# Kernel tuning notes

Hardware: AMD Instinct MI355X
Metric: run time of the kernel (lower is better)

## Reference

```python
import jax, jax.numpy as jnp
import numpy as np

B, N, D = 4, 1024, 1024
H = 16
RS, RC = 32, 32
MLP = int(D * 4.0)
EPS = 1e-6


def _ln(x):
    # LayerNorm with no scale/bias (flax defaults: eps=1e-6)
    m = jnp.mean(x, axis=-1, keepdims=True)
    v = jnp.mean(jnp.square(x - m), axis=-1, keepdims=True)
    return (x - m) * jax.lax.rsqrt(v + EPS)


def _rms(x, scale):
    rms = jnp.sqrt(jnp.mean(jnp.square(x), axis=-1, keepdims=True) + EPS)
    return scale * x / rms


def _modulate(x, shift, scale):
    return x * (1 + scale[:, None]) + shift[:, None]


def setup_inputs() -> dict:
    key = jax.random.key(0)
    ks = jax.random.split(key, 20)
    s = 0.02
    return {
        'x': jax.random.normal(ks[0], (B, N, D), jnp.float32),
        'c': jax.random.normal(ks[1], (B, D), jnp.float32),
        'cls_token': jax.random.normal(ks[2], (B, D), jnp.float32),
        'Wc': jax.random.normal(ks[3], (D, 6 * D), jnp.float32) * s,
        'bc': jax.random.normal(ks[4], (6 * D,), jnp.float32) * s,
        'Wqkv': jax.random.normal(ks[5], (D, 3 * D), jnp.float32) * s,
        'bqkv': jnp.zeros((3 * D,), jnp.float32),
        'Wo': jax.random.normal(ks[6], (D, D), jnp.float32) * s,
        'bo': jnp.zeros((D,), jnp.float32),
        'A_s': jax.random.normal(ks[7], (D, RS), jnp.float32) * s,
        'B_s': jax.random.normal(ks[8], (RS, D), jnp.float32) * s,
        'rms_s_scale': jnp.ones((D,), jnp.float32),
        'C_r': jax.random.normal(ks[9], (D, RC), jnp.float32) * s,
        'D_r': jax.random.normal(ks[10], (RC, D), jnp.float32) * s,
        'rms_c_scale': jnp.ones((D,), jnp.float32),
        'W1': jax.random.normal(ks[11], (D, MLP), jnp.float32) * s,
        'b1': jnp.zeros((MLP,), jnp.float32),
        'W2': jax.random.normal(ks[12], (MLP, D), jnp.float32) * s,
        'b2': jnp.zeros((D,), jnp.float32),
    }


def reference(x, c, cls_token, Wc, bc, Wqkv, bqkv, Wo, bo, A_s, B_s,
              rms_s_scale, C_r, D_r, rms_c_scale, W1, b1, W2, b2):
    hd = D // H
    # AdaLN conditioning
    c_proj = jax.nn.silu(c) @ Wc + bc                    # (B, 6D)
    shift_a, scale_a, gate_a, shift_m, scale_m, gate_m = jnp.split(c_proj, 6, axis=-1)

    # Self-attention branch
    x_norm = _modulate(_ln(x), shift_a, scale_a)         # (B, N, D)
    qkv = x_norm @ Wqkv + bqkv                           # (B, N, 3D)
    q, k, v = jnp.split(qkv, 3, axis=-1)
    q = q.reshape(B, N, H, hd).transpose(0, 2, 1, 3)     # (B, H, N, hd)
    k = k.reshape(B, N, H, hd).transpose(0, 2, 1, 3)
    v = v.reshape(B, N, H, hd).transpose(0, 2, 1, 3)
    attn_w = jax.nn.softmax(jnp.einsum('bhqd,bhkd->bhqk', q, k) * hd ** (-0.5), axis=-1)
    attn_out = jnp.einsum('bhqk,bhkd->bhqd', attn_w, v)
    attn_out = attn_out.transpose(0, 2, 1, 3).reshape(B, N, D)
    attn_out = attn_out @ Wo + bo
    Y = x + gate_a[:, None] * attn_out

    # Self-gram low-rank branch (residual)
    gram_s = (x @ A_s) @ B_s                             # (B, N, D)
    X_prime = _rms(gram_s, rms_s_scale) + Y

    # Cross-gram branch via CLS token (no residual)
    u_c = cls_token[:, :, None] * C_r[None]              # (B, D, RC)
    v_c = jnp.einsum('bnd,bdr->bnr', X_prime, u_c)       # (B, N, RC)
    gram_c = v_c @ D_r                                   # (B, N, D)
    Z = _rms(gram_c, rms_c_scale)

    # MLP branch
    z_norm = _modulate(_ln(Z), shift_m, scale_m)
    h = jax.nn.gelu(z_norm @ W1 + b1) @ W2 + b2
    return Z + gate_m[:, None] * h
```

## Files before the change

kernel.cpp:

```cpp
#include <hip/hip_runtime.h>
#include <stdint.h>

typedef float  f32x4  __attribute__((ext_vector_type(4)));
typedef int    i32x4  __attribute__((ext_vector_type(4)));
typedef __bf16 bf16x4 __attribute__((ext_vector_type(4)));

#define D_    1024
#define SIXD  6144
#define QSCALE 0.18033688011112042f

#define BAR() asm volatile("s_barrier" ::: "memory")

__device__ __forceinline__ void mfma16(const i32x4 &a, const i32x4 &b, f32x4 &c) {
  asm("v_mfma_f32_16x16x32_bf16 %0, %1, %2, %0" : "+v"(c) : "v"(a), "v"(b));
}
__device__ __forceinline__ void mfma16a(const i32x4 &a, const i32x4 &b, f32x4 &c) {
  asm("v_mfma_f32_16x16x32_bf16 %0, %1, %2, %0" : "+a"(c) : "v"(a), "v"(b));
}

__device__ __forceinline__ void gload_lds16(const void* g, void* l) {
  __builtin_amdgcn_global_load_lds(
      (const __attribute__((address_space(1))) uint32_t*)g,
      (__attribute__((address_space(3))) uint32_t*)l, 16, 0, 0);
}

__global__ __launch_bounds__(256)
void cond_gemm(const float* __restrict__ c, const float* __restrict__ Wc,
               const float* __restrict__ bc, float* __restrict__ cproj)
{
  __shared__ float sc[4096];
  __shared__ float tp[8][4][32];
  int tid = threadIdx.x;
  for (int i = tid; i < 4096; i += 256) {
    float v = c[i];
    sc[i] = v / (1.f + __expf(-v));
  }
  __syncthreads();
  int colo = tid & 31, kseg = tid >> 5;
  int col = blockIdx.x * 32 + colo;
  float a0 = 0.f, a1 = 0.f, a2 = 0.f, a3 = 0.f;
  for (int k = kseg * 128; k < kseg * 128 + 128; k++) {
    float w = Wc[(size_t)k * SIXD + col];
    a0 += sc[k] * w; a1 += sc[1024 + k] * w;
    a2 += sc[2048 + k] * w; a3 += sc[3072 + k] * w;
  }
  tp[kseg][0][colo] = a0; tp[kseg][1][colo] = a1;
  tp[kseg][2][colo] = a2; tp[kseg][3][colo] = a3;
  __syncthreads();
  if (kseg == 0) {
#pragma unroll
    for (int b = 0; b < 4; b++) {
      float s = bc[col];
#pragma unroll
      for (int g = 0; g < 8; g++) s += tp[g][b][colo];
      cproj[b * SIXD + col] = s;
    }
  }
}

__global__ __launch_bounds__(256)
void transpose_all(const float* __restrict__ Wqkv, const float* __restrict__ Wo,
                   const float* __restrict__ W1, const float* __restrict__ W2,
                   __bf16* __restrict__ Wqkvt, __bf16* __restrict__ Wot,
                   __bf16* __restrict__ W1t, __bf16* __restrict__ W2t)
{
  __shared__ __bf16 t[64][65];
  int bid = blockIdx.x;
  const float* W; __bf16* Wt; int Kdim, Ndim, lb;
  if (bid < 768)       { W = Wqkv; Wt = Wqkvt; Kdim = 1024; Ndim = 3072; lb = bid; }
  else if (bid < 1024) { W = Wo;   Wt = Wot;   Kdim = 1024; Ndim = 1024; lb = bid - 768; }
  else if (bid < 2048) { W = W1;   Wt = W1t;   Kdim = 1024; Ndim = 4096; lb = bid - 1024; }
  else                 { W = W2;   Wt = W2t;   Kdim = 4096; Ndim = 1024; lb = bid - 2048; }
  int ntn = Ndim >> 6;
  int kt = lb / ntn, nt = lb % ntn;
  int tid = threadIdx.x;
  const float* src = W + (size_t)(kt * 64) * Ndim + nt * 64;
#pragma unroll
  for (int i = 0; i < 4; i++) {
    int k = i * 16 + (tid >> 4);
    int c4 = tid & 15;
    float4 v = ((const float4*)(src + (size_t)k * Ndim))[c4];
    t[k][c4 * 4 + 0] = (__bf16)v.x; t[k][c4 * 4 + 1] = (__bf16)v.y;
    t[k][c4 * 4 + 2] = (__bf16)v.z; t[k][c4 * 4 + 3] = (__bf16)v.w;
  }
  __syncthreads();
  __bf16* dst = Wt + (size_t)(nt * 64) * Kdim + kt * 64;
  int n = tid >> 2, ks = (tid & 3) * 16;
  bf16x4 o0, o1, o2, o3;
#pragma unroll
  for (int j = 0; j < 4; j++) {
    o0[j] = t[ks + j][n];      o1[j] = t[ks + 4 + j][n];
    o2[j] = t[ks + 8 + j][n];  o3[j] = t[ks + 12 + j][n];
  }
  __bf16* dp = dst + (size_t)n * Kdim + ks;
  *(bf16x4*)(dp) = o0; *(bf16x4*)(dp + 4) = o1;
  *(bf16x4*)(dp + 8) = o2; *(bf16x4*)(dp + 12) = o3;
}

__global__ __launch_bounds__(256)
void transpose_v(const __bf16* __restrict__ qkv, __bf16* __restrict__ Vt)
{
  __shared__ __bf16 t[32][33];
  int bid = blockIdx.x;
  int dt = bid & 1, nt = (bid >> 1) & 31, bh = bid >> 6;
  int b = bh >> 4, h = bh & 15;
  int x = threadIdx.x & 31, yq = threadIdx.x >> 5;
  const __bf16* src = qkv + ((size_t)(b * 1024 + nt * 32)) * 3072 + 2048 + h * 64 + dt * 32;
#pragma unroll
  for (int i = 0; i < 4; i++) {
    int row = yq * 4 + i;
    t[row][x] = src[(size_t)row * 3072 + x];
  }
  __syncthreads();
  __bf16* dst = Vt + ((size_t)(bh * 64 + dt * 32)) * 1024 + nt * 32;
#pragma unroll
  for (int i = 0; i < 4; i++) {
    int drow = yq * 4 + i;
    dst[(size_t)drow * 1024 + x] = t[x][drow];
  }
}

__global__ __launch_bounds__(256)
void ln_mod(const float* __restrict__ X, const float* __restrict__ cproj,
            int shift_off, int scale_off, __bf16* __restrict__ Out)
{
  int row = blockIdx.x;
  int b = row >> 10;
  int tid = threadIdx.x;
  const float4* xr = (const float4*)(X + (size_t)row * D_);
  float4 v = xr[tid];
  float s  = v.x + v.y + v.z + v.w;
  float s2 = v.x * v.x + v.y * v.y + v.z * v.z + v.w * v.w;
#pragma unroll
  for (int off = 1; off < 64; off <<= 1) {
    s  += __shfl_xor(s,  off, 64);
    s2 += __shfl_xor(s2, off, 64);
  }
  __shared__ float red[8];
  int wave = tid >> 6, lane = tid & 63;
  if (lane == 0) { red[wave] = s; red[4 + wave] = s2; }
  __syncthreads();
  s  = red[0] + red[1] + red[2] + red[3];
  s2 = red[4] + red[5] + red[6] + red[7];
  float mean = s * (1.f / D_);
  float var  = s2 * (1.f / D_) - mean * mean;
  float rstd = rsqrtf(var + 1e-6f);
  const float4* sh = (const float4*)(cproj + b * SIXD + shift_off);
  const float4* sc = (const float4*)(cproj + b * SIXD + scale_off);
  float4 shv = sh[tid], scv = sc[tid];
  bf16x4 o;
  o[0] = (__bf16)((v.x - mean) * rstd * (1.f + scv.x) + shv.x);
  o[1] = (__bf16)((v.y - mean) * rstd * (1.f + scv.y) + shv.y);
  o[2] = (__bf16)((v.z - mean) * rstd * (1.f + scv.z) + shv.z);
  o[3] = (__bf16)((v.w - mean) * rstd * (1.f + scv.w) + shv.w);
  *(bf16x4*)(Out + (size_t)row * D_ + tid * 4) = o;
}

template<int EPI, int NBUF>
__global__ __launch_bounds__(256)
void gemm_bt(const __bf16* __restrict__ A, const __bf16* __restrict__ Bt,
             const float* __restrict__ bias, const float* __restrict__ cproj,
             int gate_off, const float* __restrict__ resid,
             void* __restrict__ Cout, void* __restrict__ Cout2,
             void* __restrict__ Cout3, void* __restrict__ Cout4,
             int M, int N, int K, int SK)
{
  __shared__ __align__(16) __bf16 As[NBUF * 128 * 32];
  __shared__ __align__(16) __bf16 Bs[NBUF * 128 * 32];
  const int PD = NBUF - 1;
  int tilesN = N >> 7, tilesM = M >> 7;
  int npersk = tilesM * tilesN;
  int sk = blockIdx.x / npersk;
  int rest = blockIdx.x % npersk;
  int cpx = npersk >> 3;
  rest = (rest & 7) * cpx + (rest >> 3);
  int bm = rest / tilesN, bn = rest % tilesN;
  int Klen = K / SK, Kstart = sk * Klen;

  int tid = threadIdx.x;
  int lane = tid & 63, wave = tid >> 6;
  int lr = lane & 15, lg = lane >> 4;
  int wm = (wave >> 1) << 6, wn = (wave & 1) << 6;

  f32x4 acc[4][4] = {};

  int sr = tid >> 2, skb = tid & 3;
  int scol = ((skb ^ ((sr >> 1) & 3)) * 8);
  const __bf16* pa = A + (size_t)((bm << 7) + sr) * K + Kstart + scol;
  const __bf16* pb = Bt + (size_t)((bn << 7) + sr) * K + Kstart + scol;
  const size_t rstep = (size_t)64 * K;
  __bf16* la = As + tid * 8;
  __bf16* lb = Bs + tid * 8;

  auto STAGE = [&](int buf, int k0) {
    int bo = buf * 4096;
    gload_lds16(pa + k0, la + bo);
    gload_lds16(pa + rstep + k0, la + bo + 2048);
    gload_lds16(pb + k0, lb + bo);
    gload_lds16(pb + rstep + k0, lb + bo + 2048);
  };

  int nt = Klen >> 5;
#pragma unroll
  for (int p = 0; p < PD; p++) STAGE(p, p * 32);

  for (int t = 0; t < nt; t++) {
    if (t + PD < nt) STAGE((t + PD) % NBUF, (t + PD) * 32);
    int ahead = nt - 1 - t; if (ahead > PD) ahead = PD;
    if (ahead >= 3)      asm volatile("s_waitcnt vmcnt(12)" ::: "memory");
    else if (ahead == 2) asm volatile("s_waitcnt vmcnt(8)" ::: "memory");
    else if (ahead == 1) asm volatile("s_waitcnt vmcnt(4)" ::: "memory");
    else                 asm volatile("s_waitcnt vmcnt(0)" ::: "memory");
    BAR();
    const __bf16* Ac = As + (t % NBUF) * 4096;
    const __bf16* Bc = Bs + (t % NBUF) * 4096;
    i32x4 af[4], bfv[4];
#pragma unroll
    for (int m = 0; m < 4; m++) {
      int row = wm + m * 16 + lr;
      af[m] = *(const i32x4*)(Ac + row * 32 + ((lg ^ ((row >> 1) & 3)) * 8));
    }
#pragma unroll
    for (int n = 0; n < 4; n++) {
      int row = wn + n * 16 + lr;
      bfv[n] = *(const i32x4*)(Bc + row * 32 + ((lg ^ ((row >> 1) & 3)) * 8));
    }
    asm volatile("s_waitcnt lgkmcnt(0)" ::: "memory");
    __builtin_amdgcn_sched_barrier(0);
    BAR();
    __builtin_amdgcn_s_setprio(1);
#pragma unroll
    for (int m = 0; m < 4; m++)
#pragma unroll
      for (int n = 0; n < 4; n++)
        mfma16(af[m], bfv[n], acc[m][n]);
    __builtin_amdgcn_s_setprio(0);
  }
  asm volatile("s_waitcnt vmcnt(0)" ::: "memory");
  asm volatile("s_nop 7\n\ts_nop 7" ::);

  __bf16* Pp = nullptr;
  if (EPI == 3) {
    if (sk == 0)      Pp = (__bf16*)Cout;
    else if (sk == 1) Pp = (__bf16*)Cout2;
    else if (sk == 2) Pp = (__bf16*)Cout3;
    else              Pp = (__bf16*)Cout4;
  }

  int row0 = (bm << 7) + wm;
  int col0 = (bn << 7) + wn;
#pragma unroll
  for (int m = 0; m < 4; m++) {
#pragma unroll
    for (int n = 0; n < 4; n++) {
      int cc = col0 + n * 16 + lr;
      float bv = (EPI == 3) ? 0.f : bias[cc];
#pragma unroll
      for (int r = 0; r < 4; r++) {
        int row = row0 + m * 16 + (lg << 2) + r;
        float v = acc[m][n][r] + bv;
        size_t idx = (size_t)row * N + cc;
        if (EPI == 0) {
          ((__bf16*)Cout)[idx] = (__bf16)v;
        } else if (EPI == 1) {
          int b = row >> 10;
          float g = cproj[b * SIXD + gate_off + cc];
          ((float*)Cout)[idx] = resid[idx] + g * v;
        } else if (EPI == 2) {
          float u = 0.7978845608028654f * (v + 0.044715f * v * v * v);
          u = fminf(fmaxf(u, -15.f), 15.f);
          float e = __expf(2.f * u);
          float th = (e - 1.f) / (e + 1.f);
          ((__bf16*)Cout)[idx] = (__bf16)(0.5f * v * (1.f + th));
        } else if (EPI == 4) {
          float scq = (cc < 1024) ? QSCALE : 1.f;
          ((__bf16*)Cout)[idx] = (__bf16)(v * scq);
        } else {
          Pp[idx] = (__bf16)v;
        }
      }
    }
  }
}

template<int EPI, int NT, int KD>
__global__ __launch_bounds__(512, 2)
void gemm256(const __bf16* __restrict__ A, const __bf16* __restrict__ Bt,
             const float* __restrict__ bias,
             void* __restrict__ Cout, void* __restrict__ Cout2,
             void* __restrict__ Cout3, void* __restrict__ Cout4,
             int M, int N)
{
  __shared__ __align__(16) __bf16 As[2 * 16384];
  __shared__ __align__(16) __bf16 Bs[2 * 16384];
  int tilesN = N >> 8, tilesM = M >> 8;
  int npersk = tilesM * tilesN;
  int sk = blockIdx.x / npersk;
  int rest = blockIdx.x % npersk;
  int cpx = npersk >> 3;
  rest = (rest & 7) * cpx + (rest >> 3);
  int bm = rest / tilesN, bn = rest % tilesN;
  int Kstart = sk * (NT * 64);

  int tid = threadIdx.x;
  int lane = tid & 63, wave = tid >> 6;
  int lr = lane & 15, lg = lane >> 4;
  int wr = wave >> 2, wc = wave & 3;

  f32x4 acc[8][4] = {};

  int srow = tid >> 3;
  int schunk = (tid & 7) ^ (srow & 7);
  const __bf16* pa = A  + (size_t)((bm << 8) + srow) * KD + Kstart + schunk * 8;
  const __bf16* pb = Bt + (size_t)((bn << 8) + srow) * KD + Kstart + schunk * 8;
  __bf16* la = As + tid * 8;
  __bf16* lb = Bs + tid * 8;

  auto SAq = [&](int t, int q) {
    gload_lds16(pa + (size_t)(q * 64) * KD + t * 64,
                la + (t & 1) * 16384 + q * 4096);
  };
  auto SBq = [&](int t, int q) {
    gload_lds16(pb + (size_t)(q * 64) * KD + t * 64,
                lb + (t & 1) * 16384 + q * 4096);
  };

#pragma unroll
  for (int q = 0; q < 4; q++) { SAq(0, q); }
#pragma unroll
  for (int q = 0; q < 4; q++) { SBq(0, q); }
#pragma unroll
  for (int q = 0; q < 4; q++) { SAq(1, q); }
#pragma unroll
  for (int q = 0; q < 4; q++) { SBq(1, q); }
  asm volatile("s_waitcnt vmcnt(8)" ::: "memory");
  BAR();

  int cc0 = ((lg ^ (lr & 7)) << 4);
  int cc1 = cc0 ^ 64;
  const char* aA = (const char*)As + (wr * 128 + lr) * 128;
  const char* aB = (const char*)Bs + (wc * 64 + lr) * 128;

  i32x4 alo[4][2], ahi[4][2], b0v[2][2], b1v[2][2];
#pragma unroll
  for (int m = 0; m < 4; m++) {
    alo[m][0] = *(const i32x4*)(aA + m * 2048 + cc0);
    alo[m][1] = *(const i32x4*)(aA + m * 2048 + cc1);
  }
#pragma unroll
  for (int n = 0; n < 2; n++) {
    b0v[n][0] = *(const i32x4*)(aB + n * 2048 + cc0);
    b0v[n][1] = *(const i32x4*)(aB + n * 2048 + cc1);
  }

  for (int t = 0; t < NT; t++) {
    const char* Ab = aA + (t & 1) * 32768;
    const char* Bb = aB + (t & 1) * 32768;

#pragma unroll
    for (int n = 0; n < 2; n++) {
      b1v[n][0] = *(const i32x4*)(Bb + 4096 + n * 2048 + cc0);
      b1v[n][1] = *(const i32x4*)(Bb + 4096 + n * 2048 + cc1);
    }
    __builtin_amdgcn_sched_barrier(0);
    __builtin_amdgcn_s_setprio(1);
#pragma unroll
    for (int m = 0; m < 4; m++)
#pragma unroll
      for (int n = 0; n < 2; n++) {
        mfma16a(alo[m][0], b0v[n][0], acc[m][n]);
        mfma16a(alo[m][1], b0v[n][1], acc[m][n]);
      }
    __builtin_amdgcn_s_setprio(0);
    asm volatile("s_waitcnt lgkmcnt(0)" ::: "memory");
    BAR();

#pragma unroll
    for (int m = 0; m < 4; m++) {
      ahi[m][0] = *(const i32x4*)(Ab + 8192 + m * 2048 + cc0);
      ahi[m][1] = *(const i32x4*)(Ab + 8192 + m * 2048 + cc1);
    }
    if (t + 2 < NT) { SBq(t + 2, 0); SBq(t + 2, 1); }
    __builtin_amdgcn_sched_barrier(0);
    __builtin_amdgcn_s_setprio(1);
#pragma unroll
    for (int m = 0; m < 4; m++)
#pragma unroll
      for (int n = 0; n < 2; n++) {
        mfma16a(alo[m][0], b1v[n][0], acc[m][2 + n]);
        mfma16a(alo[m][1], b1v[n][1], acc[m][2 + n]);
      }
    __builtin_amdgcn_s_setprio(0);
    asm volatile("s_waitcnt lgkmcnt(0)" ::: "memory");
    BAR();

    if (t + 2 < NT) {
      SBq(t + 2, 2); SBq(t + 2, 3);
      SAq(t + 2, 0); SAq(t + 2, 1); SAq(t + 2, 2); SAq(t + 2, 3);
    }
    __builtin_amdgcn_sched_barrier(0);
    __builtin_amdgcn_s_setprio(1);
#pragma unroll
    for (int m = 0; m < 4; m++)
#pragma unroll
      for (int n = 0; n < 2; n++) {
        mfma16a(ahi[m][0], b1v[n][0], acc[4 + m][2 + n]);
        mfma16a(ahi[m][1], b1v[n][1], acc[4 + m][2 + n]);
      }
#pragma unroll
    for (int m = 0; m < 4; m++)
#pragma unroll
      for (int n = 0; n < 2; n++) {
        mfma16a(ahi[m][0], b0v[n][0], acc[4 + m][n]);
        mfma16a(ahi[m][1], b0v[n][1], acc[4 + m][n]);
      }
    __builtin_amdgcn_s_setprio(0);
    if (t + 1 < NT) {
      if (t + 2 < NT) asm volatile("s_waitcnt vmcnt(8)" ::: "memory");
      else            asm volatile("s_waitcnt vmcnt(0)" ::: "memory");
      BAR();
      const char* An = aA + ((t + 1) & 1) * 32768;
      const char* Bn = aB + ((t + 1) & 1) * 32768;
#pragma unroll
      for (int m = 0; m < 4; m++) {
        alo[m][0] = *(const i32x4*)(An + m * 2048 + cc0);
        alo[m][1] = *(const i32x4*)(An + m * 2048 + cc1);
      }
#pragma unroll
      for (int n = 0; n < 2; n++) {
        b0v[n][0] = *(const i32x4*)(Bn + n * 2048 + cc0);
        b0v[n][1] = *(const i32x4*)(Bn + n * 2048 + cc1);
      }
    }
  }
  asm volatile("s_waitcnt lgkmcnt(0)" ::: "memory");
  asm volatile("s_nop 7\n\ts_nop 7" ::);

  __bf16* Pp = nullptr;
  if (EPI == 3) {
    if (sk == 0)      Pp = (__bf16*)Cout;
    else if (sk == 1) Pp = (__bf16*)Cout2;
    else if (sk == 2) Pp = (__bf16*)Cout3;
    else              Pp = (__bf16*)Cout4;
  }

  int row0 = (bm << 8) + wr * 128;
  int col0 = (bn << 8) + wc * 64;
#pragma unroll
  for (int m = 0; m < 8; m++) {
#pragma unroll
    for (int n = 0; n < 4; n++) {
      int cc = col0 + n * 16 + lr;
      float bv = (EPI == 3) ? 0.f : bias[cc];
#pragma unroll
      for (int r = 0; r < 4; r++) {
        int row = row0 + m * 16 + (lg << 2) + r;
        float v = acc[m][n][r] + bv;
        size_t idx = (size_t)row * N + cc;
        if (EPI == 2) {
          float u = 0.7978845608028654f * (v + 0.044715f * v * v * v);
          u = fminf(fmaxf(u, -15.f), 15.f);
          float e = __expf(2.f * u);
          float th = (e - 1.f) / (e + 1.f);
          ((__bf16*)Cout)[idx] = (__bf16)(0.5f * v * (1.f + th));
        } else if (EPI == 4) {
          float scq = (cc < 1024) ? QSCALE : 1.f;
          ((__bf16*)Cout)[idx] = (__bf16)(v * scq);
        } else {
          Pp[idx] = (__bf16)v;
        }
      }
    }
  }
}

__global__ __launch_bounds__(256)
void reduce_w2(const __bf16* __restrict__ P0, const __bf16* __restrict__ P1,
               const __bf16* __restrict__ P2, const __bf16* __restrict__ P3,
               const float* __restrict__ bias, const float* __restrict__ cproj,
               float* __restrict__ Out)
{
  int row = blockIdx.x;
  int b = row >> 10;
  int tid = threadIdx.x;
  size_t base = (size_t)row * D_ + tid * 4;
  bf16x4 a0 = *(const bf16x4*)(P0 + base);
  bf16x4 a1 = *(const bf16x4*)(P1 + base);
  bf16x4 a2 = *(const bf16x4*)(P2 + base);
  bf16x4 a3 = *(const bf16x4*)(P3 + base);
  f32x4 s;
#pragma unroll
  for (int i = 0; i < 4; i++)
    s[i] = ((float)a0[i] + (float)a1[i]) + ((float)a2[i] + (float)a3[i]);
  f32x4 bz = *(const f32x4*)(bias + tid * 4);
  f32x4 g  = *(const f32x4*)(cproj + b * SIXD + 5120 + tid * 4);
  f32x4 z  = *(const f32x4*)(Out + base);
  *(f32x4*)(Out + base) = z + g * (s + bz);
}

__global__ __launch_bounds__(512, 4)
void attn_flash(const __bf16* __restrict__ qkv, const __bf16* __restrict__ Vt,
                __bf16* __restrict__ O)
{
  __shared__ __align__(16) __bf16 Kl[2][64 * 64];
  __shared__ __align__(16) __bf16 Vl[2][64 * 64];
  __shared__ __align__(16) __bf16 Pl[8][16 * 64];

  int bid = ((blockIdx.x & 7) << 6) | (blockIdx.x >> 3);
  int qt = bid & 7, h = (bid >> 3) & 15, b = bid >> 7;
  int tid = threadIdx.x, wave = tid >> 6, lane = tid & 63;
  int lr = lane & 15, lg = lane >> 4;

  size_t tok0 = (size_t)b * 1024;
  int qrow = qt * 128 + wave * 16 + lr;
  const __bf16* qptr = qkv + (tok0 + qrow) * 3072 + h * 64;
  i32x4 qf0 = *(const i32x4*)(qptr + lg * 8);
  i32x4 qf1 = *(const i32x4*)(qptr + 32 + lg * 8);

  float l_acc[4] = {0.f, 0.f, 0.f, 0.f};
  f32x4 oacc[4] = {};

  const __bf16* kbase = qkv + tok0 * 3072 + 1024 + h * 64;
  const __bf16* vbase = Vt + ((size_t)(b * 16 + h) * 64) * 1024;

  int skey = tid >> 3, sdb = tid & 7;
  const __bf16* ksrc = kbase + (size_t)skey * 3072 + ((sdb ^ (skey & 7)) * 8);
  const __bf16* vsrc = vbase + (size_t)skey * 1024 + ((sdb ^ (skey & 7)) * 8);
  __bf16* klp = &Kl[0][0] + tid * 8;
  __bf16* vlp = &Vl[0][0] + tid * 8;
  __bf16* pl = &Pl[wave][0];

  auto STAGE = [&](int buf, int kk) {
    gload_lds16(ksrc + (size_t)kk * 3072, klp + buf * 4096);
    gload_lds16(vsrc + kk, vlp + buf * 4096);
  };

  STAGE(0, 0);
  int cur = 0;
  for (int k0 = 0; k0 < 1024; k0 += 64) {
    int kn = (k0 + 64 < 1024) ? (k0 + 64) : k0;
    STAGE(cur ^ 1, kn);
    asm volatile("s_waitcnt vmcnt(2)" ::: "memory");
    BAR();
    const __bf16* K_ = &Kl[cur][0];
    const __bf16* V_ = &Vl[cur][0];

    f32x4 s[4];
    __builtin_amdgcn_s_setprio(1);
#pragma unroll
    for (int n = 0; n < 4; n++) {
      int key = n * 16 + lr;
      int kx = key & 7;
      i32x4 kf0 = *(const i32x4*)(K_ + key * 64 + ((lg ^ kx) * 8));
      i32x4 kf1 = *(const i32x4*)(K_ + key * 64 + (((4 + lg) ^ kx) * 8));
      f32x4 sa = {0.f, 0.f, 0.f, 0.f};
      mfma16(qf0, kf0, sa);
      mfma16(qf1, kf1, sa);
      s[n] = sa;
    }
    __builtin_amdgcn_s_setprio(0);

#pragma unroll
    for (int n = 0; n < 4; n++)
#pragma unroll
      for (int r = 0; r < 4; r++)
        s[n][r] = exp2f(s[n][r]);
#pragma unroll
    for (int r = 0; r < 4; r++)
      l_acc[r] += (s[0][r] + s[1][r]) + (s[2][r] + s[3][r]);

#pragma unroll
    for (int n = 0; n < 4; n++)
#pragma unroll
      for (int r = 0; r < 4; r++) {
        int prow = lg * 4 + r;
        int key = n * 16 + lr;
        int idx = prow * 64 + (((key >> 3) ^ (prow & 7)) * 8) + (key & 7);
        pl[idx] = (__bf16)s[n][r];
      }
    asm volatile("s_waitcnt lgkmcnt(0)" ::: "memory");
    __builtin_amdgcn_sched_barrier(0);
    i32x4 pf0 = *(const i32x4*)(pl + lr * 64 + ((lg ^ (lr & 7)) * 8));
    i32x4 pf1 = *(const i32x4*)(pl + lr * 64 + (((4 + lg) ^ (lr & 7)) * 8));

    __builtin_amdgcn_s_setprio(1);
#pragma unroll
    for (int dt = 0; dt < 4; dt++) {
      int vrow = dt * 16 + lr, rx = vrow & 7;
      i32x4 vf0 = *(const i32x4*)(V_ + vrow * 64 + ((lg ^ rx) * 8));
      i32x4 vf1 = *(const i32x4*)(V_ + vrow * 64 + (((4 + lg) ^ rx) * 8));
      mfma16(pf0, vf0, oacc[dt]);
      mfma16(pf1, vf1, oacc[dt]);
    }
    __builtin_amdgcn_s_setprio(0);
    asm volatile("s_waitcnt lgkmcnt(0)" ::: "memory");
    __builtin_amdgcn_sched_barrier(0);
    BAR();
    cur ^= 1;
  }
  asm volatile("s_waitcnt vmcnt(0)" ::: "memory");
  asm volatile("s_nop 7\n\ts_nop 7" ::);

  float rinv[4];
#pragma unroll
  for (int r = 0; r < 4; r++) {
    float v = l_acc[r];
#pragma unroll
    for (int off = 1; off < 16; off <<= 1) v += __shfl_xor(v, off, 64);
    rinv[r] = 1.f / v;
  }

  int orow = qt * 128 + wave * 16 + (lg << 2);
#pragma unroll
  for (int dt = 0; dt < 4; dt++)
#pragma unroll
    for (int r = 0; r < 4; r++) {
      float v = oacc[dt][r] * rinv[r];
      O[(tok0 + orow + r) * 1024 + h * 64 + dt * 16 + lr] = (__bf16)v;
    }
}

__global__ __launch_bounds__(256)
void gram_fused(const float* __restrict__ X, const float* __restrict__ Y,
                const float* __restrict__ cls,
                const float* __restrict__ A_s, const float* __restrict__ B_s,
                const float* __restrict__ rms_s,
                const float* __restrict__ C_r, const float* __restrict__ D_r,
                const float* __restrict__ rms_c,
                const float* __restrict__ cproj,
                float* __restrict__ Z, __bf16* __restrict__ Znorm)
{
  __shared__ float xs[4][D_];
  __shared__ float tp[8][4][32];
  __shared__ float t1[4][32];
  __shared__ float red[4][4];
  __shared__ float red2[4][4][2];
  int row0 = blockIdx.x * 4;
  int b = row0 >> 10;
  int tid = threadIdx.x;
  int wv = tid >> 6;

  f32x4 cv = *(const f32x4*)(cls + (size_t)b * D_ + tid * 4);
  f32x4 yv[4];
#pragma unroll
  for (int rr = 0; rr < 4; rr++) {
    ((f32x4*)xs[rr])[tid] = *(const f32x4*)(X + (size_t)(row0 + rr) * D_ + tid * 4);
    yv[rr] = *(const f32x4*)(Y + (size_t)(row0 + rr) * D_ + tid * 4);
  }
  __syncthreads();

  {
    int r = tid & 31, seg = tid >> 5;
    float a0 = 0.f, a1 = 0.f, a2 = 0.f, a3 = 0.f;
    const float* ap = A_s + r;
    for (int d = seg * 128; d < seg * 128 + 128; d++) {
      float w = ap[d * 32];
      a0 += xs[0][d] * w; a1 += xs[1][d] * w;
      a2 += xs[2][d] * w; a3 += xs[3][d] * w;
    }
    tp[seg][0][r] = a0; tp[seg][1][r] = a1; tp[seg][2][r] = a2; tp[seg][3][r] = a3;
  }
  __syncthreads();
  if (tid < 128) {
    int rr = tid >> 5, r = tid & 31;
    float sv = 0.f;
#pragma unroll
    for (int g = 0; g < 8; g++) sv += tp[g][rr][r];
    t1[rr][r] = sv;
  }
  __syncthreads();

  f32x4 g[4] = {};
  for (int r = 0; r < 32; r++) {
    f32x4 bv = *(const f32x4*)(B_s + (size_t)r * D_ + tid * 4);
    g[0] += t1[0][r] * bv; g[1] += t1[1][r] * bv;
    g[2] += t1[2][r] * bv; g[3] += t1[3][r] * bv;
  }
  float ssl[4];
#pragma unroll
  for (int rr = 0; rr < 4; rr++)
    ssl[rr] = g[rr][0]*g[rr][0] + g[rr][1]*g[rr][1] + g[rr][2]*g[rr][2] + g[rr][3]*g[rr][3];
#pragma unroll
  for (int off = 1; off < 64; off <<= 1)
#pragma unroll
    for (int rr = 0; rr < 4; rr++) ssl[rr] += __shfl_xor(ssl[rr], off, 64);
  if ((tid & 63) == 0) {
#pragma unroll
    for (int rr = 0; rr < 4; rr++) red[wv][rr] = ssl[rr];
  }
  __syncthreads();
  {
    f32x4 scv = *(const f32x4*)(rms_s + tid * 4);
#pragma unroll
    for (int rr = 0; rr < 4; rr++) {
      float ss = red[0][rr] + red[1][rr] + red[2][rr] + red[3][rr];
      float rs = rsqrtf(ss * (1.f / D_) + 1e-6f);
      f32x4 xp = scv * g[rr] * rs + yv[rr];
      ((f32x4*)xs[rr])[tid] = xp * cv;
    }
  }
  __syncthreads();

  {
    int r = tid & 31, seg = tid >> 5;
    float a0 = 0.f, a1 = 0.f, a2 = 0.f, a3 = 0.f;
    const float* cp = C_r + r;
    for (int d = seg * 128; d < seg * 128 + 128; d++) {
      float w = cp[d * 32];
      a0 += xs[0][d] * w; a1 += xs[1][d] * w;
      a2 += xs[2][d] * w; a3 += xs[3][d] * w;
    }
    tp[seg][0][r] = a0; tp[seg][1][r] = a1; tp[seg][2][r] = a2; tp[seg][3][r] = a3;
  }
  __syncthreads();
  if (tid < 128) {
    int rr = tid >> 5, r = tid & 31;
    float sv = 0.f;
#pragma unroll
    for (int g2i = 0; g2i < 8; g2i++) sv += tp[g2i][rr][r];
    t1[rr][r] = sv;
  }
  __syncthreads();

  f32x4 g2[4] = {};
  for (int r = 0; r < 32; r++) {
    f32x4 bv = *(const f32x4*)(D_r + (size_t)r * D_ + tid * 4);
    g2[0] += t1[0][r] * bv; g2[1] += t1[1][r] * bv;
    g2[2] += t1[2][r] * bv; g2[3] += t1[3][r] * bv;
  }
#pragma unroll
  for (int rr = 0; rr < 4; rr++)
    ssl[rr] = g2[rr][0]*g2[rr][0] + g2[rr][1]*g2[rr][1] + g2[rr][2]*g2[rr][2] + g2[rr][3]*g2[rr][3];
#pragma unroll
  for (int off = 1; off < 64; off <<= 1)
#pragma unroll
    for (int rr = 0; rr < 4; rr++) ssl[rr] += __shfl_xor(ssl[rr], off, 64);
  if ((tid & 63) == 0) {
#pragma unroll
    for (int rr = 0; rr < 4; rr++) red[wv][rr] = ssl[rr];
  }
  __syncthreads();
  f32x4 z[4];
  {
    f32x4 scv = *(const f32x4*)(rms_c + tid * 4);
#pragma unroll
    for (int rr = 0; rr < 4; rr++) {
      float ss = red[0][rr] + red[1][rr] + red[2][rr] + red[3][rr];
      float rs = rsqrtf(ss * (1.f / D_) + 1e-6f);
      z[rr] = scv * g2[rr] * rs;
    }
  }

  float s1l[4], s2l[4];
#pragma unroll
  for (int rr = 0; rr < 4; rr++) {
    s1l[rr] = z[rr][0] + z[rr][1] + z[rr][2] + z[rr][3];
    s2l[rr] = z[rr][0]*z[rr][0] + z[rr][1]*z[rr][1] + z[rr][2]*z[rr][2] + z[rr][3]*z[rr][3];
  }
#pragma unroll
  for (int off = 1; off < 64; off <<= 1)
#pragma unroll
    for (int rr = 0; rr < 4; rr++) {
      s1l[rr] += __shfl_xor(s1l[rr], off, 64);
      s2l[rr] += __shfl_xor(s2l[rr], off, 64);
    }
  if ((tid & 63) == 0) {
#pragma unroll
    for (int rr = 0; rr < 4; rr++) { red2[wv][rr][0] = s1l[rr]; red2[wv][rr][1] = s2l[rr]; }
  }
  __syncthreads();
  f32x4 shv = *(const f32x4*)(cproj + b * SIXD + 3072 + tid * 4);
  f32x4 scm = *(const f32x4*)(cproj + b * SIXD + 4096 + tid * 4);
#pragma unroll
  for (int rr = 0; rr < 4; rr++) {
    float S  = red2[0][rr][0] + red2[1][rr][0] + red2[2][rr][0] + red2[3][rr][0];
    float S2 = red2[0][rr][1] + red2[1][rr][1] + red2[2][rr][1] + red2[3][rr][1];
    float mean = S * (1.f / D_);
    float var  = S2 * (1.f / D_) - mean * mean;
    float rstd = rsqrtf(var + 1e-6f);
    f32x4 zn = (z[rr] - mean) * rstd * (scm + 1.f) + shv;
    *(f32x4*)(Z + (size_t)(row0 + rr) * D_ + tid * 4) = z[rr];
    bf16x4 o;
#pragma unroll
    for (int i = 0; i < 4; i++) o[i] = (__bf16)zn[i];
    *(bf16x4*)(Znorm + (size_t)(row0 + rr) * D_ + tid * 4) = o;
  }
}

extern "C" void kernel_launch(void* const* d_in, const int* in_sizes, int n_in,
                              void* d_out, int out_size, void* d_ws, size_t ws_size,
                              hipStream_t stream)
{
  const float* x     = (const float*)d_in[0];
  const float* c     = (const float*)d_in[1];
  const float* cls   = (const float*)d_in[2];
  const float* Wc    = (const float*)d_in[3];
  const float* bc    = (const float*)d_in[4];
  const float* Wqkv  = (const float*)d_in[5];
  const float* bqkv  = (const float*)d_in[6];
  const float* Wo    = (const float*)d_in[7];
  const float* bo    = (const float*)d_in[8];
  const float* A_s   = (const float*)d_in[9];
  const float* B_s   = (const float*)d_in[10];
  const float* rms_s = (const float*)d_in[11];
  const float* C_r   = (const float*)d_in[12];
  const float* D_r   = (const float*)d_in[13];
  const float* rms_c = (const float*)d_in[14];
  const float* W1    = (const float*)d_in[15];
  const float* b1    = (const float*)d_in[16];
  const float* W2    = (const float*)d_in[17];
  const float* b2    = (const float*)d_in[18];
  float* out = (float*)d_out;

  float* ws = (float*)d_ws;
  __bf16* Wqkvt = (__bf16*)(ws + 0);
  __bf16* Wot   = (__bf16*)(ws + 1572864);
  __bf16* W1t   = (__bf16*)(ws + 2097152);
  __bf16* W2t   = (__bf16*)(ws + 4194304);
  float*  cproj = ws + 6291456;
  __bf16* xnorm = (__bf16*)(ws + 6316032);
  __bf16* qkv   = (__bf16*)(ws + 8413184);
  __bf16* Vt    = (__bf16*)(ws + 14704640);
  __bf16* h1    = (__bf16*)(ws + 8413184);
  __bf16* attno = (__bf16*)(ws + 16801792);
  float*  Ybuf  = ws + 18898944;
  __bf16* P0 = (__bf16*)(ws + 0);
  __bf16* P1 = (__bf16*)(ws + 2097152);
  __bf16* P2 = (__bf16*)(ws + 16801792);
  __bf16* P3 = (__bf16*)(ws + 18898944);

  cond_gemm<<<192, 256, 0, stream>>>(c, Wc, bc, cproj);
  transpose_all<<<3072, 256, 0, stream>>>(Wqkv, Wo, W1, W2, Wqkvt, Wot, W1t, W2t);
  ln_mod<<<4096, 256, 0, stream>>>(x, cproj, 0, 1024, xnorm);
  gemm256<4, 16, 1024><<<192, 512, 0, stream>>>(xnorm, Wqkvt, bqkv,
                                                qkv, nullptr, nullptr, nullptr,
                                                4096, 3072);
  transpose_v<<<4096, 256, 0, stream>>>(qkv, Vt);
  attn_flash<<<512, 512, 0, stream>>>(qkv, Vt, attno);
  gemm_bt<1, 4><<<256, 256, 0, stream>>>(attno, Wot, bo, cproj, 2048, x,
                                         Ybuf, nullptr, nullptr, nullptr,
                                         4096, 1024, 1024, 1);
  gram_fused<<<1024, 256, 0, stream>>>(x, Ybuf, cls, A_s, B_s, rms_s,
                                       C_r, D_r, rms_c, cproj, out, xnorm);
  gemm256<2, 16, 1024><<<256, 512, 0, stream>>>(xnorm, W1t, b1,
                                                h1, nullptr, nullptr, nullptr,
                                                4096, 4096);
  gemm256<3, 16, 4096><<<256, 512, 0, stream>>>(h1, W2t, nullptr,
                                                P0, P1, P2, P3, 4096, 1024);
  reduce_w2<<<4096, 256, 0, stream>>>(P0, P1, P2, P3, b2, cproj, out);
}
```

Before: 265.1 us.

## Restructure GEMM main loop into four barrier-separated phases with staggered prefetch

```diff
diff --git a/kernel.cpp b/kernel.cpp
--- a/kernel.cpp
+++ b/kernel.cpp
@@ -325,15 +325,11 @@
                 lb + (t & 1) * 16384 + q * 4096);
   };
 
-#pragma unroll
-  for (int q = 0; q < 4; q++) { SAq(0, q); }
-#pragma unroll
-  for (int q = 0; q < 4; q++) { SBq(0, q); }
-#pragma unroll
-  for (int q = 0; q < 4; q++) { SAq(1, q); }
-#pragma unroll
-  for (int q = 0; q < 4; q++) { SBq(1, q); }
-  asm volatile("s_waitcnt vmcnt(8)" ::: "memory");
+  SAq(0, 0); SAq(0, 1); SAq(0, 2); SAq(0, 3);
+  SBq(0, 0); SBq(0, 1); SBq(0, 2); SBq(0, 3);
+  SAq(1, 0); SAq(1, 2);
+  SBq(1, 0); SBq(1, 1); SBq(1, 2); SBq(1, 3);
+  asm volatile("s_waitcnt vmcnt(6)" ::: "memory");
   BAR();
 
   int cc0 = ((lg ^ (lr & 7)) << 4);
@@ -341,99 +337,97 @@
   const char* aA = (const char*)As + (wr * 128 + lr) * 128;
   const char* aB = (const char*)Bs + (wc * 64 + lr) * 128;
 
-  i32x4 alo[4][2], ahi[4][2], b0v[2][2], b1v[2][2];
-#pragma unroll
-  for (int m = 0; m < 4; m++) {
-    alo[m][0] = *(const i32x4*)(aA + m * 2048 + cc0);
-    alo[m][1] = *(const i32x4*)(aA + m * 2048 + cc1);
-  }
-#pragma unroll
-  for (int n = 0; n < 2; n++) {
-    b0v[n][0] = *(const i32x4*)(aB + n * 2048 + cc0);
-    b0v[n][1] = *(const i32x4*)(aB + n * 2048 + cc1);
-  }
-
+  i32x4 av[4][2], b0v[2][2], b1v[2][2];
+
+#pragma unroll 2
   for (int t = 0; t < NT; t++) {
     const char* Ab = aA + (t & 1) * 32768;
     const char* Bb = aB + (t & 1) * 32768;
 
 #pragma unroll
+    for (int m = 0; m < 4; m++) {
+      av[m][0] = *(const i32x4*)(Ab + m * 2048 + cc0);
+      av[m][1] = *(const i32x4*)(Ab + m * 2048 + cc1);
+    }
+#pragma unroll
+    for (int n = 0; n < 2; n++) {
+      b0v[n][0] = *(const i32x4*)(Bb + n * 2048 + cc0);
+      b0v[n][1] = *(const i32x4*)(Bb + n * 2048 + cc1);
+    }
+    if (t + 1 < NT) { SAq(t + 1, 1); SAq(t + 1, 3); }
+    asm volatile("s_waitcnt lgkmcnt(8)" ::: "memory");
+    BAR();
+    asm volatile("s_waitcnt lgkmcnt(0)" ::: "memory");
+    __builtin_amdgcn_sched_barrier(0);
+    __builtin_amdgcn_s_setprio(1);
+#pragma unroll
+    for (int m = 0; m < 4; m++)
+#pragma unroll
+      for (int n = 0; n < 2; n++) {
+        mfma16a(av[m][0], b0v[n][0], acc[m][n]);
+        mfma16a(av[m][1], b0v[n][1], acc[m][n]);
+      }
+    __builtin_amdgcn_s_setprio(0);
+    BAR();
+
+#pragma unroll
     for (int n = 0; n < 2; n++) {
       b1v[n][0] = *(const i32x4*)(Bb + 4096 + n * 2048 + cc0);
       b1v[n][1] = *(const i32x4*)(Bb + 4096 + n * 2048 + cc1);
     }
+    if (t + 2 < NT) { SAq(t + 2, 0); SAq(t + 2, 2); }
+    BAR();
+    asm volatile("s_waitcnt lgkmcnt(0)" ::: "memory");
     __builtin_amdgcn_sched_barrier(0);
     __builtin_amdgcn_s_setprio(1);
 #pragma unroll
     for (int m = 0; m < 4; m++)
 #pragma unroll
       for (int n = 0; n < 2; n++) {
-        mfma16a(alo[m][0], b0v[n][0], acc[m][n]);
-        mfma16a(alo[m][1], b0v[n][1], acc[m][n]);
+        mfma16a(av[m][0], b1v[n][0], acc[m][2 + n]);
+        mfma16a(av[m][1], b1v[n][1], acc[m][2 + n]);
       }
     __builtin_amdgcn_s_setprio(0);
+    BAR();
+
+#pragma unroll
+    for (int m = 0; m < 4; m++) {
+      av[m][0] = *(const i32x4*)(Ab + 8192 + m * 2048 + cc0);
+      av[m][1] = *(const i32x4*)(Ab + 8192 + m * 2048 + cc1);
+    }
+    if (t + 2 < NT) { SBq(t + 2, 0); SBq(t + 2, 1); }
+    BAR();
     asm volatile("s_waitcnt lgkmcnt(0)" ::: "memory");
-    BAR();
-
-#pragma unroll
-    for (int m = 0; m < 4; m++) {
-      ahi[m][0] = *(const i32x4*)(Ab + 8192 + m * 2048 + cc0);
-      ahi[m][1] = *(const i32x4*)(Ab + 8192 + m * 2048 + cc1);
-    }
-    if (t + 2 < NT) { SBq(t + 2, 0); SBq(t + 2, 1); }
     __builtin_amdgcn_sched_barrier(0);
     __builtin_amdgcn_s_setprio(1);
 #pragma unroll
     for (int m = 0; m < 4; m++)
 #pragma unroll
       for (int n = 0; n < 2; n++) {
-        mfma16a(alo[m][0], b1v[n][0], acc[m][2 + n]);
-        mfma16a(alo[m][1], b1v[n][1], acc[m][2 + n]);
+        mfma16a(av[m][0], b1v[n][0], acc[4 + m][2 + n]);
+        mfma16a(av[m][1], b1v[n][1], acc[4 + m][2 + n]);
       }
     __builtin_amdgcn_s_setprio(0);
-    asm volatile("s_waitcnt lgkmcnt(0)" ::: "memory");
     BAR();
 
     if (t + 2 < NT) {
       SBq(t + 2, 2); SBq(t + 2, 3);
-      SAq(t + 2, 0); SAq(t + 2, 1); SAq(t + 2, 2); SAq(t + 2, 3);
-    }
-    __builtin_amdgcn_sched_barrier(0);
+      asm volatile("s_waitcnt vmcnt(6)" ::: "memory");
+    } else {
+      asm volatile("s_waitcnt vmcnt(0)" ::: "memory");
+    }
+    BAR();
     __builtin_amdgcn_s_setprio(1);
 #pragma unroll
     for (int m = 0; m < 4; m++)
 #pragma unroll
       for (int n = 0; n < 2; n++) {
-        mfma16a(ahi[m][0], b1v[n][0], acc[4 + m][2 + n]);
-        mfma16a(ahi[m][1], b1v[n][1], acc[4 + m][2 + n]);
-      }
-#pragma unroll
-    for (int m = 0; m < 4; m++)
-#pragma unroll
-      for (int n = 0; n < 2; n++) {
-        mfma16a(ahi[m][0], b0v[n][0], acc[4 + m][n]);
-        mfma16a(ahi[m][1], b0v[n][1], acc[4 + m][n]);
+        mfma16a(av[m][0], b0v[n][0], acc[4 + m][n]);
+        mfma16a(av[m][1], b0v[n][1], acc[4 + m][n]);
       }
     __builtin_amdgcn_s_setprio(0);
-    if (t + 1 < NT) {
-      if (t + 2 < NT) asm volatile("s_waitcnt vmcnt(8)" ::: "memory");
-      else            asm volatile("s_waitcnt vmcnt(0)" ::: "memory");
-      BAR();
-      const char* An = aA + ((t + 1) & 1) * 32768;
-      const char* Bn = aB + ((t + 1) & 1) * 32768;
-#pragma unroll
-      for (int m = 0; m < 4; m++) {
-        alo[m][0] = *(const i32x4*)(An + m * 2048 + cc0);
-        alo[m][1] = *(const i32x4*)(An + m * 2048 + cc1);
-      }
-#pragma unroll
-      for (int n = 0; n < 2; n++) {
-        b0v[n][0] = *(const i32x4*)(Bn + n * 2048 + cc0);
-        b0v[n][1] = *(const i32x4*)(Bn + n * 2048 + cc1);
-      }
-    }
-  }
-  asm volatile("s_waitcnt lgkmcnt(0)" ::: "memory");
+    BAR();
+  }
   asm volatile("s_nop 7\n\ts_nop 7" ::);
 
   __bf16* Pp = nullptr;
```

New measurement: 337.4 us. 27.3% more time.
